# Performance work log

Measured on AMD Instinct MI355X. Metric: run time of the kernel, lower is better.

## Reference

```python
import jax, jax.numpy as jnp
import numpy as np
from jax import lax

B, L, D, C = 4096, 50, 128, 64
V = 100000
H = D // 2  # bidirectional LSTM hidden size; 2*H == emb_dim


def setup_inputs() -> dict:
    key = jax.random.key(0)
    ks = jax.random.split(key, 26)
    f = lambda k, s: jax.random.normal(k, s, dtype=jnp.float32) * 0.05
    return {
        "r_idx": jax.random.randint(ks[0], (B,), 0, V),
        "a_idx": jax.random.randint(ks[1], (B,), 0, V),
        "acc_idx": jax.random.randint(ks[2], (B,), 0, V),
        "rank_q": jax.random.normal(ks[3], (B, L, D), dtype=jnp.float32),
        "rank_q_len": jax.random.randint(ks[4], (B,), 0, L),
        "ru_emb": f(ks[5], (V, D)),
        "au_emb": f(ks[6], (V, D)),
        "Wih_f": f(ks[7], (4 * H, D)), "Whh_f": f(ks[8], (4 * H, H)),
        "bih_f": f(ks[9], (4 * H,)), "bhh_f": f(ks[10], (4 * H,)),
        "Wih_b": f(ks[11], (4 * H, D)), "Whh_b": f(ks[12], (4 * H, H)),
        "bih_b": f(ks[13], (4 * H,)), "bhh_b": f(ks[14], (4 * H,)),
        "conv1_w": f(ks[15], (C, 1, D)), "conv1_b": f(ks[16], (C,)),
        "conv2_w": f(ks[17], (C, 2, D)), "conv2_b": f(ks[18], (C,)),
        "conv3_w": f(ks[19], (C, 3, D)), "conv3_b": f(ks[20], (C,)),
        "fc1_w": f(ks[21], (6,)), "fc1_b": f(ks[22], (1,)),
        "fc2_w": f(ks[23], (C,)), "fc2_b": f(ks[24], (1,)),
    }


def _lstm_dir(x, Wih, Whh, bih, bhh, reverse):
    # x: [B, L, D] -> outputs [B, L, H]; PyTorch gate order i,f,g,o
    b = x.shape[0]
    xs = jnp.swapaxes(x, 0, 1)  # [L, B, D]
    h0 = jnp.zeros((b, Whh.shape[1]), x.dtype)

    def step(carry, xt):
        h, c = carry
        gates = xt @ Wih.T + h @ Whh.T + (bih + bhh)
        i, fg, g, o = jnp.split(gates, 4, axis=-1)
        i = jax.nn.sigmoid(i)
        fg = jax.nn.sigmoid(fg)
        g = jnp.tanh(g)
        o = jax.nn.sigmoid(o)
        c = fg * c + i * g
        h = o * jnp.tanh(c)
        return (h, c), h

    _, ys = lax.scan(step, (h0, h0), xs, reverse=reverse)
    return jnp.swapaxes(ys, 0, 1)


def _score(mat, conv1_w, conv1_b, conv2_w, conv2_b, conv3_w, conv3_b, fc1_w, fc1_b, fc2_w, fc2_b):
    # mat: [B, 3, D]; three tiny conv branches (kernel heights 1/2/3, width=D)
    branches = []
    for w, bias in ((conv1_w, conv1_b), (conv2_w, conv2_b), (conv3_w, conv3_b)):
        k = w.shape[1]
        wins = jnp.stack([mat[:, i:i + k] for i in range(3 - k + 1)], axis=1)  # [B, W, k, D]
        branches.append(jax.nn.relu(jnp.einsum('bwkd,ckd->bcw', wins, w) + bias[None, :, None]))
    s = jnp.concatenate(branches, axis=2)  # [B, C, 6]
    h = jnp.einsum('bcw,w->bc', s, fc1_w) + fc1_b[0]  # fc_new_1: 6 -> 1
    return jnp.einsum('bc,c->b', h, fc2_w) + fc2_b[0]  # fc_new_2: C -> 1


def reference(r_idx, a_idx, acc_idx, rank_q, rank_q_len, ru_emb, au_emb,
              Wih_f, Whh_f, bih_f, bhh_f, Wih_b, Whh_b, bih_b, bhh_b,
              conv1_w, conv1_b, conv2_w, conv2_b, conv3_w, conv3_b,
              fc1_w, fc1_b, fc2_w, fc2_b):
    emb_r = ru_emb[r_idx]
    emb_a = au_emb[a_idx]
    emb_acc = au_emb[acc_idx]
    # bidirectional LSTM over the question sequence
    out_f = _lstm_dir(rank_q, Wih_f, Whh_f, bih_f, bhh_f, reverse=False)
    out_b = _lstm_dir(rank_q, Wih_b, Whh_b, bih_b, bhh_b, reverse=True)
    q_out = jnp.concatenate([out_f, out_b], axis=-1)  # [B, L, D]
    # prepend a zero timestep, then gather per-example at index rank_q_len
    q_pad = jnp.concatenate([jnp.zeros((q_out.shape[0], 1, q_out.shape[2]), q_out.dtype), q_out], axis=1)
    emb_q = q_pad[jnp.arange(q_pad.shape[0]), rank_q_len]  # [B, D]
    low = jnp.stack([emb_r, emb_q, emb_a], axis=1)   # [B, 3, D]
    high = jnp.stack([emb_r, emb_q, emb_acc], axis=1)
    fcp = (conv1_w, conv1_b, conv2_w, conv2_b, conv3_w, conv3_b, fc1_w, fc1_b, fc2_w, fc2_b)
    low_s = _score(low, *fcp)
    high_s = _score(high, *fcp)
    return jnp.sum(low_s - high_s)
```

## Files before the change

kernel.cpp:

```cpp
#include <hip/hip_runtime.h>
#include <hip/hip_bf16.h>

#define LSEQ 50
#define BATCH 4096

typedef __attribute__((ext_vector_type(8))) short bf16x8;
typedef __attribute__((ext_vector_type(4))) float f32x4;

__device__ __forceinline__ unsigned cvtpk(float lo, float hi) {
    unsigned r;
    asm("v_cvt_pk_bf16_f32 %0, %1, %2" : "=v"(r) : "v"(lo), "v"(hi));
    return r;
}
__device__ __forceinline__ bf16x8 pack8(float4 a, float4 b) {
    uint4 u;
    u.x = cvtpk(a.x, a.y); u.y = cvtpk(a.z, a.w);
    u.z = cvtpk(b.x, b.y); u.w = cvtpk(b.z, b.w);
    return __builtin_bit_cast(bf16x8, u);
}
__device__ __forceinline__ float fsigm(float x) {
    return __builtin_amdgcn_rcpf(1.0f + __builtin_amdgcn_exp2f(-1.44269504f * x));
}
__device__ __forceinline__ float ftanh(float x) {
    float e = __builtin_amdgcn_exp2f(2.88539008f * x);
    return 1.0f - 2.0f * __builtin_amdgcn_rcpf(e + 1.0f);
}

__global__ __launch_bounds__(256, 2)
void lstm_kernel(const float* __restrict__ rank_q, const int* __restrict__ qlen,
                 const float* __restrict__ Wih_f, const float* __restrict__ Whh_f,
                 const float* __restrict__ bih_f, const float* __restrict__ bhh_f,
                 const float* __restrict__ Wih_b, const float* __restrict__ Whh_b,
                 const float* __restrict__ bih_b, const float* __restrict__ bhh_b,
                 float* __restrict__ embq)
{
    const int blk = blockIdx.x;
    const int dir = blk >> 8;
    const int b0  = (blk & 255) << 4;
    const int tid = threadIdx.x;
    const int wv  = tid >> 6;
    const int ln  = tid & 63;
    const int lm  = ln & 15;
    const int lq  = ln >> 4;
    const int m   = (wv << 4) + lm;

    const float* Wih = dir ? Wih_b : Wih_f;
    const float* Whh = dir ? Whh_b : Whh_f;
    const float* bih = dir ? bih_b : bih_f;
    const float* bhh = dir ? bhh_b : bhh_f;

    __shared__ __align__(16) unsigned short xbuf[3][16][136];
    __shared__ __align__(16) unsigned short hbuf[2][16][72];

    bf16x8 bfrag[4][6];
    float bias[4];
    #pragma unroll
    for (int j = 0; j < 4; ++j) {
        const int n = (j << 6) + m;
        bias[j] = bih[n] + bhh[n];
        #pragma unroll
        for (int s = 0; s < 6; ++s) {
            const int kb = (s << 5) + (lq << 3);
            const float* src = (s < 4) ? (Wih + n * 128 + kb)
                                       : (Whh + n * 64 + (kb - 128));
            bfrag[j][s] = pack8(*(const float4*)src, *(const float4*)(src + 4));
        }
    }

    int len_e[4];
    #pragma unroll
    for (int r = 0; r < 4; ++r) len_e[r] = qlen[b0 + (lq << 2) + r];

    float cst[4]  = {0.f, 0.f, 0.f, 0.f};
    float qval[4] = {0.f, 0.f, 0.f, 0.f};

    for (int i = tid; i < 16 * 72; i += 256) ((unsigned short*)hbuf)[i] = 0;

    const int se = tid >> 4;
    const int sd = (tid & 15) << 3;
    const int tstep = dir ? -128 : 128;
    const float* gp = rank_q + ((size_t)(b0 + se) * LSEQ + (dir ? LSEQ - 1 : 0)) * 128 + sd;

    {
        float4 a0 = *(const float4*)gp, b0v = *(const float4*)(gp + 4); gp += tstep;
        float4 a1 = *(const float4*)gp, b1v = *(const float4*)(gp + 4); gp += tstep;
        *(bf16x8*)&xbuf[0][se][sd] = pack8(a0, b0v);
        *(bf16x8*)&xbuf[1][se][sd] = pack8(a1, b1v);
    }
    __syncthreads();

    const int xoff = lm * 136 + (lq << 3);
    const int hoff = lm * 72 + (lq << 3);

    f32x4 accx[4];
    {
        const unsigned short* xb = &xbuf[0][0][0];
        bf16x8 x0 = *(const bf16x8*)(xb + xoff);
        bf16x8 x1 = *(const bf16x8*)(xb + xoff + 32);
        bf16x8 x2 = *(const bf16x8*)(xb + xoff + 64);
        bf16x8 x3 = *(const bf16x8*)(xb + xoff + 96);
        #pragma unroll
        for (int j = 0; j < 4; ++j) {
            f32x4 a = {bias[j], bias[j], bias[j], bias[j]};
            a = __builtin_amdgcn_mfma_f32_16x16x32_bf16(x0, bfrag[j][0], a, 0, 0, 0);
            a = __builtin_amdgcn_mfma_f32_16x16x32_bf16(x1, bfrag[j][1], a, 0, 0, 0);
            a = __builtin_amdgcn_mfma_f32_16x16x32_bf16(x2, bfrag[j][2], a, 0, 0, 0);
            a = __builtin_amdgcn_mfma_f32_16x16x32_bf16(x3, bfrag[j][3], a, 0, 0, 0);
            accx[j] = a;
        }
    }

    int r1 = 1, w2 = 2;
    for (int it = 0; it < LSEQ; ++it) {
        const int t   = dir ? (LSEQ - 1 - it) : it;
        const int rbh = it & 1;
        const int wbh = rbh ^ 1;

        float4 nxa, nxb;
        const bool pf = (it <= LSEQ - 3);
        if (pf) { nxa = *(const float4*)gp; nxb = *(const float4*)(gp + 4); gp += tstep; }

        const unsigned short* hb = &hbuf[rbh][0][0];
        bf16x8 ah0 = *(const bf16x8*)(hb + hoff);
        bf16x8 ah1 = *(const bf16x8*)(hb + hoff + 32);
        f32x4 gate[4];
        #pragma unroll
        for (int j = 0; j < 4; ++j) {
            f32x4 a = __builtin_amdgcn_mfma_f32_16x16x32_bf16(ah0, bfrag[j][4], accx[j], 0, 0, 0);
            gate[j]  = __builtin_amdgcn_mfma_f32_16x16x32_bf16(ah1, bfrag[j][5], a, 0, 0, 0);
        }

        if (it + 1 < LSEQ) {
            const unsigned short* xb = &xbuf[r1][0][0];
            bf16x8 x0 = *(const bf16x8*)(xb + xoff);
            bf16x8 x1 = *(const bf16x8*)(xb + xoff + 32);
            bf16x8 x2 = *(const bf16x8*)(xb + xoff + 64);
            bf16x8 x3 = *(const bf16x8*)(xb + xoff + 96);
            #pragma unroll
            for (int j = 0; j < 4; ++j) {
                f32x4 a = {bias[j], bias[j], bias[j], bias[j]};
                a = __builtin_amdgcn_mfma_f32_16x16x32_bf16(x0, bfrag[j][0], a, 0, 0, 0);
                a = __builtin_amdgcn_mfma_f32_16x16x32_bf16(x1, bfrag[j][1], a, 0, 0, 0);
                a = __builtin_amdgcn_mfma_f32_16x16x32_bf16(x2, bfrag[j][2], a, 0, 0, 0);
                a = __builtin_amdgcn_mfma_f32_16x16x32_bf16(x3, bfrag[j][3], a, 0, 0, 0);
                accx[j] = a;
            }
        }

        float hn[4];
        #pragma unroll
        for (int r = 0; r < 4; ++r) {
            float ig = fsigm(gate[0][r]);
            float fg = fsigm(gate[1][r]);
            float gg = ftanh(gate[2][r]);
            float og = fsigm(gate[3][r]);
            float cn = fg * cst[r] + ig * gg;
            cst[r] = cn;
            hn[r] = og * ftanh(cn);
            if (t == len_e[r] - 1) qval[r] = hn[r];
        }
        const unsigned u01 = cvtpk(hn[0], hn[1]);
        const unsigned u23 = cvtpk(hn[2], hn[3]);
        hbuf[wbh][(lq << 2) + 0][m] = (unsigned short)u01;
        hbuf[wbh][(lq << 2) + 1][m] = (unsigned short)(u01 >> 16);
        hbuf[wbh][(lq << 2) + 2][m] = (unsigned short)u23;
        hbuf[wbh][(lq << 2) + 3][m] = (unsigned short)(u23 >> 16);

        if (pf) *(bf16x8*)&xbuf[w2][se][sd] = pack8(nxa, nxb);

        __syncthreads();
        r1 = (r1 == 2) ? 0 : r1 + 1;
        w2 = (w2 == 2) ? 0 : w2 + 1;
    }

    #pragma unroll
    for (int r = 0; r < 4; ++r)
        embq[(size_t)(b0 + (lq << 2) + r) * 128 + (dir << 6) + m] = qval[r];
}

__global__ __launch_bounds__(256)
void prep_kernel(const float* __restrict__ c1w, const float* __restrict__ c2w,
                 const float* __restrict__ c3w, float* __restrict__ T)
{
    const int id = blockIdx.x * 256 + threadIdx.x;
    const int m  = id >> 13;
    const int rem = id & 8191;
    const int j  = rem >> 8;
    const int q  = rem & 255;
    const int c  = q >> 2;
    const int d  = (j << 2) + (q & 3);
    const float* src;
    switch (m) {
        case 0:  src = c1w + c * 128 + d;       break;
        case 1:  src = c2w + c * 256 + d;       break;
        case 2:  src = c2w + c * 256 + 128 + d; break;
        case 3:  src = c3w + c * 384 + d;       break;
        case 4:  src = c3w + c * 384 + 128 + d; break;
        default: src = c3w + c * 384 + 256 + d; break;
    }
    T[id] = *src;
}

__global__ __launch_bounds__(256)
void score_kernel(const int* __restrict__ r_idx, const int* __restrict__ a_idx,
                  const int* __restrict__ acc_idx,
                  const float* __restrict__ ru, const float* __restrict__ au,
                  const float* __restrict__ embq, const float* __restrict__ T,
                  const float* __restrict__ c1b, const float* __restrict__ c2b,
                  const float* __restrict__ c3b,
                  const float* __restrict__ fc1w, const float* __restrict__ fc2w,
                  float* __restrict__ diff)
{
    const int tid = threadIdx.x;
    const int wv  = tid >> 6;
    const int c   = tid & 63;
    const int b0  = blockIdx.x << 4;

    __shared__ __align__(16) float emb[64][132];
    {
        const int row = tid & 63;
        const int e   = row >> 2, v = row & 3;
        const int seg = (tid >> 6) << 5;
        const int bb  = b0 + e;
        const float* src = (v == 0) ? ru   + (size_t)r_idx[bb]   * 128 :
                           (v == 1) ? embq + (size_t)bb          * 128 :
                           (v == 2) ? au   + (size_t)a_idx[bb]   * 128 :
                                      au   + (size_t)acc_idx[bb] * 128;
        #pragma unroll
        for (int i = 0; i < 8; ++i) {
            float4 x = *(const float4*)(src + seg + (i << 2));
            *(float4*)&emb[row][seg + (i << 2)] = x;
        }
    }
    __syncthreads();

    float acc[4][9];
    #pragma unroll
    for (int e = 0; e < 4; ++e)
        #pragma unroll
        for (int k = 0; k < 9; ++k) acc[e][k] = 0.f;

    const float4* Tq = (const float4*)T;
    for (int j = 0; j < 32; ++j) {
        const float4* wq = Tq + j * 64 + c;
        const float4 w1  = wq[0];
        const float4 w20 = wq[2048];
        const float4 w21 = wq[4096];
        const float4 w30 = wq[6144];
        const float4 w31 = wq[8192];
        const float4 w32 = wq[10240];
        const int jd = j << 2;
        #pragma unroll
        for (int e = 0; e < 4; ++e) {
            const int br = ((wv << 2) + e) << 2;
            const float4 er = *(const float4*)&emb[br + 0][jd];
            const float4 eq = *(const float4*)&emb[br + 1][jd];
            const float4 ea = *(const float4*)&emb[br + 2][jd];
            const float4 ex = *(const float4*)&emb[br + 3][jd];
            acc[e][0] += w1.x*ea.x  + w1.y*ea.y  + w1.z*ea.z  + w1.w*ea.w;
            acc[e][1] += w1.x*ex.x  + w1.y*ex.y  + w1.z*ex.z  + w1.w*ex.w;
            acc[e][2] += w20.x*eq.x + w20.y*eq.y + w20.z*eq.z + w20.w*eq.w;
            acc[e][3] += w21.x*ea.x + w21.y*ea.y + w21.z*ea.z + w21.w*ea.w;
            acc[e][4] += w21.x*ex.x + w21.y*ex.y + w21.z*ex.z + w21.w*ex.w;
            acc[e][5] += w30.x*er.x + w30.y*er.y + w30.z*er.z + w30.w*er.w;
            acc[e][6] += w31.x*eq.x + w31.y*eq.y + w31.z*eq.z + w31.w*eq.w;
            acc[e][7] += w32.x*ea.x + w32.y*ea.y + w32.z*ea.z + w32.w*ea.w;
            acc[e][8] += w32.x*ex.x + w32.y*ex.y + w32.z*ex.z + w32.w*ex.w;
        }
    }

    const float b1 = c1b[c], b2 = c2b[c], b3 = c3b[c], f2 = fc2w[c];
    const float f12 = fc1w[2], f14 = fc1w[4], f15 = fc1w[5];
    #pragma unroll
    for (int e = 0; e < 4; ++e) {
        const float r1 = fmaxf(acc[e][0] + b1, 0.f) - fmaxf(acc[e][1] + b1, 0.f);
        const float r2 = fmaxf(acc[e][2] + acc[e][3] + b2, 0.f)
                       - fmaxf(acc[e][2] + acc[e][4] + b2, 0.f);
        const float r3 = fmaxf(acc[e][5] + acc[e][6] + acc[e][7] + b3, 0.f)
                       - fmaxf(acc[e][5] + acc[e][6] + acc[e][8] + b3, 0.f);
        float term = f2 * (f12 * r1 + f14 * r2 + f15 * r3);
        #pragma unroll
        for (int off = 32; off; off >>= 1) term += __shfl_down(term, off);
        if (c == 0) diff[b0 + (wv << 2) + e] = term;
    }
}

__global__ void reduce_kernel(const float* __restrict__ diff, float* __restrict__ out)
{
    __shared__ float s[256];
    const int tid = threadIdx.x;
    float v = 0.f;
    for (int i = tid; i < BATCH; i += 256) v += diff[i];
    s[tid] = v;
    __syncthreads();
    for (int st = 128; st > 0; st >>= 1) {
        if (tid < st) s[tid] += s[tid + st];
        __syncthreads();
    }
    if (tid == 0) out[0] = s[0];
}

extern "C" void kernel_launch(void* const* d_in, const int* in_sizes, int n_in,
                              void* d_out, int out_size, void* d_ws, size_t ws_size,
                              hipStream_t stream) {
    (void)in_sizes; (void)n_in; (void)out_size; (void)ws_size;
    const int*   r_idx   = (const int*)d_in[0];
    const int*   a_idx   = (const int*)d_in[1];
    const int*   acc_idx = (const int*)d_in[2];
    const float* rank_q  = (const float*)d_in[3];
    const int*   qlen    = (const int*)d_in[4];
    const float* ru      = (const float*)d_in[5];
    const float* au      = (const float*)d_in[6];
    const float* Wih_f   = (const float*)d_in[7];
    const float* Whh_f   = (const float*)d_in[8];
    const float* bih_f   = (const float*)d_in[9];
    const float* bhh_f   = (const float*)d_in[10];
    const float* Wih_b   = (const float*)d_in[11];
    const float* Whh_b   = (const float*)d_in[12];
    const float* bih_b   = (const float*)d_in[13];
    const float* bhh_b   = (const float*)d_in[14];
    const float* c1w     = (const float*)d_in[15];
    const float* c1b     = (const float*)d_in[16];
    const float* c2w     = (const float*)d_in[17];
    const float* c2b     = (const float*)d_in[18];
    const float* c3w     = (const float*)d_in[19];
    const float* c3b     = (const float*)d_in[20];
    const float* fc1w    = (const float*)d_in[21];
    const float* fc2w    = (const float*)d_in[23];

    float* embq = (float*)d_ws;
    float* diff = embq + (size_t)BATCH * 128;
    float* T    = diff + BATCH;

    prep_kernel<<<192, 256, 0, stream>>>(c1w, c2w, c3w, T);
    lstm_kernel<<<512, 256, 0, stream>>>(rank_q, qlen, Wih_f, Whh_f, bih_f, bhh_f,
                                         Wih_b, Whh_b, bih_b, bhh_b, embq);
    score_kernel<<<BATCH / 16, 256, 0, stream>>>(r_idx, a_idx, acc_idx, ru, au, embq, T,
                                                 c1b, c2b, c3b, fc1w, fc2w, diff);
    reduce_kernel<<<1, 256, 0, stream>>>(diff, (float*)d_out);
}
```

Measured before the change: 96.77 us.

## Sort batch by sequence length and truncate LSTM steps per group

A single-block counting sort orders batch elements by qlen, and each LSTM block handles 16 elements of similar length. The forward direction runs only up to the group's maximum length, and the backward direction runs only as far back as the smallest nonzero length. Blocks are interleaved short/long across the grid to balance load. Because only the hidden state at index len-1 is consumed, the skipped timesteps are never needed, so total recurrent work drops to roughly half. The cost is an extra serial sort kernel launch, gathered row loads of rank_q, and a scattered write of embq.

```diff
diff --git a/kernel.cpp b/kernel.cpp
--- a/kernel.cpp
+++ b/kernel.cpp
@@ -26,8 +26,29 @@
     return 1.0f - 2.0f * __builtin_amdgcn_rcpf(e + 1.0f);
 }
 
+__global__ __launch_bounds__(256)
+void sort_kernel(const int* __restrict__ qlen, int* __restrict__ perm)
+{
+    __shared__ int base[64];
+    const int tid = threadIdx.x;
+    if (tid < 64) base[tid] = 0;
+    __syncthreads();
+    for (int i = tid; i < BATCH; i += 256) atomicAdd(&base[qlen[i]], 1);
+    __syncthreads();
+    if (tid == 0) {
+        int s = 0;
+        for (int v = 0; v < 50; ++v) { int c = base[v]; base[v] = s; s += c; }
+    }
+    __syncthreads();
+    for (int i = tid; i < BATCH; i += 256) {
+        int pos = atomicAdd(&base[qlen[i]], 1);
+        perm[pos] = i;
+    }
+}
+
 __global__ __launch_bounds__(256, 2)
 void lstm_kernel(const float* __restrict__ rank_q, const int* __restrict__ qlen,
+                 const int* __restrict__ perm,
                  const float* __restrict__ Wih_f, const float* __restrict__ Whh_f,
                  const float* __restrict__ bih_f, const float* __restrict__ bhh_f,
                  const float* __restrict__ Wih_b, const float* __restrict__ Whh_b,
@@ -36,7 +57,9 @@
 {
     const int blk = blockIdx.x;
     const int dir = blk >> 8;
-    const int b0  = (blk & 255) << 4;
+    const int bb  = blk & 255;
+    const int grp = (bb & 1) ? (255 - (bb >> 1)) : (bb >> 1);
+    const int b0  = grp << 4;
     const int tid = threadIdx.x;
     const int wv  = tid >> 6;
     const int ln  = tid & 63;
@@ -51,6 +74,10 @@
 
     __shared__ __align__(16) unsigned short xbuf[3][16][136];
     __shared__ __align__(16) unsigned short hbuf[2][16][72];
+    __shared__ int len_s[16];
+
+    if (tid < 16) len_s[tid] = qlen[perm[b0 + tid]];
+    for (int i = tid; i < 16 * 72; i += 256) ((unsigned short*)hbuf)[i] = 0;
 
     bf16x8 bfrag[4][6];
     float bias[4];
@@ -67,71 +94,54 @@
         }
     }
 
-    int len_e[4];
-    #pragma unroll
-    for (int r = 0; r < 4; ++r) len_e[r] = qlen[b0 + (lq << 2) + r];
+    int exq[4], len_e[4];
+    #pragma unroll
+    for (int r = 0; r < 4; ++r) {
+        exq[r]   = perm[b0 + (lq << 2) + r];
+        len_e[r] = qlen[exq[r]];
+    }
 
     float cst[4]  = {0.f, 0.f, 0.f, 0.f};
     float qval[4] = {0.f, 0.f, 0.f, 0.f};
 
-    for (int i = tid; i < 16 * 72; i += 256) ((unsigned short*)hbuf)[i] = 0;
-
-    const int se = tid >> 4;
-    const int sd = (tid & 15) << 3;
+    const int se  = tid >> 4;
+    const int exs = perm[b0 + se];
+    const int sd  = (tid & 15) << 3;
     const int tstep = dir ? -128 : 128;
-    const float* gp = rank_q + ((size_t)(b0 + se) * LSEQ + (dir ? LSEQ - 1 : 0)) * 128 + sd;
-
-    {
-        float4 a0 = *(const float4*)gp, b0v = *(const float4*)(gp + 4); gp += tstep;
-        float4 a1 = *(const float4*)gp, b1v = *(const float4*)(gp + 4); gp += tstep;
-        *(bf16x8*)&xbuf[0][se][sd] = pack8(a0, b0v);
-        *(bf16x8*)&xbuf[1][se][sd] = pack8(a1, b1v);
-    }
-    __syncthreads();
-
-    const int xoff = lm * 136 + (lq << 3);
-    const int hoff = lm * 72 + (lq << 3);
-
-    f32x4 accx[4];
-    {
-        const unsigned short* xb = &xbuf[0][0][0];
-        bf16x8 x0 = *(const bf16x8*)(xb + xoff);
-        bf16x8 x1 = *(const bf16x8*)(xb + xoff + 32);
-        bf16x8 x2 = *(const bf16x8*)(xb + xoff + 64);
-        bf16x8 x3 = *(const bf16x8*)(xb + xoff + 96);
-        #pragma unroll
-        for (int j = 0; j < 4; ++j) {
-            f32x4 a = {bias[j], bias[j], bias[j], bias[j]};
-            a = __builtin_amdgcn_mfma_f32_16x16x32_bf16(x0, bfrag[j][0], a, 0, 0, 0);
-            a = __builtin_amdgcn_mfma_f32_16x16x32_bf16(x1, bfrag[j][1], a, 0, 0, 0);
-            a = __builtin_amdgcn_mfma_f32_16x16x32_bf16(x2, bfrag[j][2], a, 0, 0, 0);
-            a = __builtin_amdgcn_mfma_f32_16x16x32_bf16(x3, bfrag[j][3], a, 0, 0, 0);
-            accx[j] = a;
-        }
-    }
-
-    int r1 = 1, w2 = 2;
-    for (int it = 0; it < LSEQ; ++it) {
-        const int t   = dir ? (LSEQ - 1 - it) : it;
-        const int rbh = it & 1;
-        const int wbh = rbh ^ 1;
-
-        float4 nxa, nxb;
-        const bool pf = (it <= LSEQ - 3);
-        if (pf) { nxa = *(const float4*)gp; nxb = *(const float4*)(gp + 4); gp += tstep; }
-
-        const unsigned short* hb = &hbuf[rbh][0][0];
-        bf16x8 ah0 = *(const bf16x8*)(hb + hoff);
-        bf16x8 ah1 = *(const bf16x8*)(hb + hoff + 32);
-        f32x4 gate[4];
-        #pragma unroll
-        for (int j = 0; j < 4; ++j) {
-            f32x4 a = __builtin_amdgcn_mfma_f32_16x16x32_bf16(ah0, bfrag[j][4], accx[j], 0, 0, 0);
-            gate[j]  = __builtin_amdgcn_mfma_f32_16x16x32_bf16(ah1, bfrag[j][5], a, 0, 0, 0);
-        }
-
-        if (it + 1 < LSEQ) {
-            const unsigned short* xb = &xbuf[r1][0][0];
+    const float* gp = rank_q + ((size_t)exs * LSEQ + (dir ? LSEQ - 1 : 0)) * 128 + sd;
+
+    __syncthreads();
+
+    int steps;
+    if (dir == 0) {
+        int mx = 0;
+        #pragma unroll
+        for (int i = 0; i < 16; ++i) mx = max(mx, len_s[i]);
+        steps = mx;
+    } else {
+        int mn = 51;
+        #pragma unroll
+        for (int i = 0; i < 16; ++i) { int l = len_s[i]; mn = min(mn, l ? l : 51); }
+        steps = (mn == 51) ? 0 : 51 - mn;
+    }
+
+    if (steps > 0) {
+        {
+            float4 a0 = *(const float4*)gp, b0v = *(const float4*)(gp + 4); gp += tstep;
+            float4 a1 = *(const float4*)gp, b1v = *(const float4*)(gp + 4); gp += tstep;
+            *(bf16x8*)&xbuf[0][se][sd] = pack8(a0, b0v);
+            *(bf16x8*)&xbuf[1][se][sd] = pack8(a1, b1v);
+        }
+        float4 ha, hb2;
+        if (3 <= steps) { ha = *(const float4*)gp; hb2 = *(const float4*)(gp + 4); gp += tstep; }
+        __syncthreads();
+
+        const int xoff = lm * 136 + (lq << 3);
+        const int hoff = lm * 72 + (lq << 3);
+
+        f32x4 accx[4];
+        {
+            const unsigned short* xb = &xbuf[0][0][0];
             bf16x8 x0 = *(const bf16x8*)(xb + xoff);
             bf16x8 x1 = *(const bf16x8*)(xb + xoff + 32);
             bf16x8 x2 = *(const bf16x8*)(xb + xoff + 64);
@@ -147,35 +157,74 @@
             }
         }
 
-        float hn[4];
-        #pragma unroll
-        for (int r = 0; r < 4; ++r) {
-            float ig = fsigm(gate[0][r]);
-            float fg = fsigm(gate[1][r]);
-            float gg = ftanh(gate[2][r]);
-            float og = fsigm(gate[3][r]);
-            float cn = fg * cst[r] + ig * gg;
-            cst[r] = cn;
-            hn[r] = og * ftanh(cn);
-            if (t == len_e[r] - 1) qval[r] = hn[r];
-        }
-        const unsigned u01 = cvtpk(hn[0], hn[1]);
-        const unsigned u23 = cvtpk(hn[2], hn[3]);
-        hbuf[wbh][(lq << 2) + 0][m] = (unsigned short)u01;
-        hbuf[wbh][(lq << 2) + 1][m] = (unsigned short)(u01 >> 16);
-        hbuf[wbh][(lq << 2) + 2][m] = (unsigned short)u23;
-        hbuf[wbh][(lq << 2) + 3][m] = (unsigned short)(u23 >> 16);
-
-        if (pf) *(bf16x8*)&xbuf[w2][se][sd] = pack8(nxa, nxb);
-
-        __syncthreads();
-        r1 = (r1 == 2) ? 0 : r1 + 1;
-        w2 = (w2 == 2) ? 0 : w2 + 1;
+        int r1 = 1, w2 = 2;
+        for (int it = 0; it < steps; ++it) {
+            const int t   = dir ? (LSEQ - 1 - it) : it;
+            const int rbh = it & 1;
+            const int wbh = rbh ^ 1;
+
+            float4 na, nb;
+            const bool nv = (it + 4 <= steps);
+            if (nv) { na = *(const float4*)gp; nb = *(const float4*)(gp + 4); gp += tstep; }
+
+            const unsigned short* hb = &hbuf[rbh][0][0];
+            bf16x8 ah0 = *(const bf16x8*)(hb + hoff);
+            bf16x8 ah1 = *(const bf16x8*)(hb + hoff + 32);
+            f32x4 gate[4];
+            #pragma unroll
+            for (int j = 0; j < 4; ++j) {
+                f32x4 a = __builtin_amdgcn_mfma_f32_16x16x32_bf16(ah0, bfrag[j][4], accx[j], 0, 0, 0);
+                gate[j]  = __builtin_amdgcn_mfma_f32_16x16x32_bf16(ah1, bfrag[j][5], a, 0, 0, 0);
+            }
+
+            if (it + 1 < steps) {
+                const unsigned short* xb = &xbuf[r1][0][0];
+                bf16x8 x0 = *(const bf16x8*)(xb + xoff);
+                bf16x8 x1 = *(const bf16x8*)(xb + xoff + 32);
+                bf16x8 x2 = *(const bf16x8*)(xb + xoff + 64);
+                bf16x8 x3 = *(const bf16x8*)(xb + xoff + 96);
+                #pragma unroll
+                for (int j = 0; j < 4; ++j) {
+                    f32x4 a = {bias[j], bias[j], bias[j], bias[j]};
+                    a = __builtin_amdgcn_mfma_f32_16x16x32_bf16(x0, bfrag[j][0], a, 0, 0, 0);
+                    a = __builtin_amdgcn_mfma_f32_16x16x32_bf16(x1, bfrag[j][1], a, 0, 0, 0);
+                    a = __builtin_amdgcn_mfma_f32_16x16x32_bf16(x2, bfrag[j][2], a, 0, 0, 0);
+                    a = __builtin_amdgcn_mfma_f32_16x16x32_bf16(x3, bfrag[j][3], a, 0, 0, 0);
+                    accx[j] = a;
+                }
+            }
+
+            float hn[4];
+            #pragma unroll
+            for (int r = 0; r < 4; ++r) {
+                float ig = fsigm(gate[0][r]);
+                float fg = fsigm(gate[1][r]);
+                float gg = ftanh(gate[2][r]);
+                float og = fsigm(gate[3][r]);
+                float cn = fg * cst[r] + ig * gg;
+                cst[r] = cn;
+                hn[r] = og * ftanh(cn);
+                if (t == len_e[r] - 1) qval[r] = hn[r];
+            }
+            const unsigned u01 = cvtpk(hn[0], hn[1]);
+            const unsigned u23 = cvtpk(hn[2], hn[3]);
+            hbuf[wbh][(lq << 2) + 0][m] = (unsigned short)u01;
+            hbuf[wbh][(lq << 2) + 1][m] = (unsigned short)(u01 >> 16);
+            hbuf[wbh][(lq << 2) + 2][m] = (unsigned short)u23;
+            hbuf[wbh][(lq << 2) + 3][m] = (unsigned short)(u23 >> 16);
+
+            if (it + 3 <= steps) *(bf16x8*)&xbuf[w2][se][sd] = pack8(ha, hb2);
+            ha = na; hb2 = nb;
+
+            __syncthreads();
+            r1 = (r1 == 2) ? 0 : r1 + 1;
+            w2 = (w2 == 2) ? 0 : w2 + 1;
+        }
     }
 
     #pragma unroll
     for (int r = 0; r < 4; ++r)
-        embq[(size_t)(b0 + (lq << 2) + r) * 128 + (dir << 6) + m] = qval[r];
+        embq[(size_t)exq[r] * 128 + (dir << 6) + m] = qval[r];
 }
 
 __global__ __launch_bounds__(256)
@@ -331,9 +380,12 @@
     float* embq = (float*)d_ws;
     float* diff = embq + (size_t)BATCH * 128;
     float* T    = diff + BATCH;
-
+    int*   perm = (int*)(T + 49152);
+
+    sort_kernel<<<1, 256, 0, stream>>>(qlen, perm);
     prep_kernel<<<192, 256, 0, stream>>>(c1w, c2w, c3w, T);
-    lstm_kernel<<<512, 256, 0, stream>>>(rank_q, qlen, Wih_f, Whh_f, bih_f, bhh_f,
+    lstm_kernel<<<512, 256, 0, stream>>>(rank_q, qlen, perm,
+                                         Wih_f, Whh_f, bih_f, bhh_f,
                                          Wih_b, Whh_b, bih_b, bhh_b, embq);
     score_kernel<<<BATCH / 16, 256, 0, stream>>>(r_idx, a_idx, acc_idx, ru, au, embq, T,
                                                  c1b, c2b, c3b, fc1w, fc2w, diff);
```

After: 95.26 us. Within noise of the previous version (-1.6%).

## Deepen rank_q prefetch ring and use raw barrier in LSTM recurrence

Applied to the files above, without the earlier changes.

The shared x staging ring grows from 3 to 4 slots. Two register-held prefetch sets now keep global loads of rank_q about six timesteps ahead, and the time loop is manually unrolled by two through a macro. The per-step __syncthreads is replaced with an inline `s_waitcnt lgkmcnt(0); s_barrier`, so the barrier waits only on LDS traffic and in-flight global loads are not drained every step. This aims to hide global load latency behind the serial recurrence, at the cost of more registers and more LDS per block.

```diff
diff --git a/kernel.cpp b/kernel.cpp
--- a/kernel.cpp
+++ b/kernel.cpp
@@ -49,7 +49,7 @@
     const float* bih = dir ? bih_b : bih_f;
     const float* bhh = dir ? bhh_b : bhh_f;
 
-    __shared__ __align__(16) unsigned short xbuf[3][16][136];
+    __shared__ __align__(16) unsigned short xbuf[4][16][136];
     __shared__ __align__(16) unsigned short hbuf[2][16][72];
 
     bf16x8 bfrag[4][6];
@@ -81,12 +81,16 @@
     const int tstep = dir ? -128 : 128;
     const float* gp = rank_q + ((size_t)(b0 + se) * LSEQ + (dir ? LSEQ - 1 : 0)) * 128 + sd;
 
-    {
-        float4 a0 = *(const float4*)gp, b0v = *(const float4*)(gp + 4); gp += tstep;
-        float4 a1 = *(const float4*)gp, b1v = *(const float4*)(gp + 4); gp += tstep;
-        *(bf16x8*)&xbuf[0][se][sd] = pack8(a0, b0v);
-        *(bf16x8*)&xbuf[1][se][sd] = pack8(a1, b1v);
-    }
+    float4 p0a = *(const float4*)gp, p0b = *(const float4*)(gp + 4); gp += tstep;
+    float4 p1a = *(const float4*)gp, p1b = *(const float4*)(gp + 4); gp += tstep;
+    float4 p2a = *(const float4*)gp, p2b = *(const float4*)(gp + 4); gp += tstep;
+    float4 p3a = *(const float4*)gp, p3b = *(const float4*)(gp + 4); gp += tstep;
+    float4 fa0 = *(const float4*)gp, fa1 = *(const float4*)(gp + 4); gp += tstep;
+    float4 fb0 = *(const float4*)gp, fb1 = *(const float4*)(gp + 4); gp += tstep;
+    *(bf16x8*)&xbuf[0][se][sd] = pack8(p0a, p0b);
+    *(bf16x8*)&xbuf[1][se][sd] = pack8(p1a, p1b);
+    *(bf16x8*)&xbuf[2][se][sd] = pack8(p2a, p2b);
+    *(bf16x8*)&xbuf[3][se][sd] = pack8(p3a, p3b);
     __syncthreads();
 
     const int xoff = lm * 136 + (lq << 3);
@@ -110,68 +114,75 @@
         }
     }
 
-    int r1 = 1, w2 = 2;
-    for (int it = 0; it < LSEQ; ++it) {
-        const int t   = dir ? (LSEQ - 1 - it) : it;
-        const int rbh = it & 1;
-        const int wbh = rbh ^ 1;
-
-        float4 nxa, nxb;
-        const bool pf = (it <= LSEQ - 3);
-        if (pf) { nxa = *(const float4*)gp; nxb = *(const float4*)(gp + 4); gp += tstep; }
-
-        const unsigned short* hb = &hbuf[rbh][0][0];
-        bf16x8 ah0 = *(const bf16x8*)(hb + hoff);
-        bf16x8 ah1 = *(const bf16x8*)(hb + hoff + 32);
-        f32x4 gate[4];
-        #pragma unroll
-        for (int j = 0; j < 4; ++j) {
-            f32x4 a = __builtin_amdgcn_mfma_f32_16x16x32_bf16(ah0, bfrag[j][4], accx[j], 0, 0, 0);
-            gate[j]  = __builtin_amdgcn_mfma_f32_16x16x32_bf16(ah1, bfrag[j][5], a, 0, 0, 0);
-        }
-
-        if (it + 1 < LSEQ) {
-            const unsigned short* xb = &xbuf[r1][0][0];
-            bf16x8 x0 = *(const bf16x8*)(xb + xoff);
-            bf16x8 x1 = *(const bf16x8*)(xb + xoff + 32);
-            bf16x8 x2 = *(const bf16x8*)(xb + xoff + 64);
-            bf16x8 x3 = *(const bf16x8*)(xb + xoff + 96);
-            #pragma unroll
-            for (int j = 0; j < 4; ++j) {
-                f32x4 a = {bias[j], bias[j], bias[j], bias[j]};
-                a = __builtin_amdgcn_mfma_f32_16x16x32_bf16(x0, bfrag[j][0], a, 0, 0, 0);
-                a = __builtin_amdgcn_mfma_f32_16x16x32_bf16(x1, bfrag[j][1], a, 0, 0, 0);
-                a = __builtin_amdgcn_mfma_f32_16x16x32_bf16(x2, bfrag[j][2], a, 0, 0, 0);
-                a = __builtin_amdgcn_mfma_f32_16x16x32_bf16(x3, bfrag[j][3], a, 0, 0, 0);
-                accx[j] = a;
-            }
-        }
-
-        float hn[4];
-        #pragma unroll
-        for (int r = 0; r < 4; ++r) {
-            float ig = fsigm(gate[0][r]);
-            float fg = fsigm(gate[1][r]);
-            float gg = ftanh(gate[2][r]);
-            float og = fsigm(gate[3][r]);
-            float cn = fg * cst[r] + ig * gg;
-            cst[r] = cn;
-            hn[r] = og * ftanh(cn);
-            if (t == len_e[r] - 1) qval[r] = hn[r];
-        }
-        const unsigned u01 = cvtpk(hn[0], hn[1]);
-        const unsigned u23 = cvtpk(hn[2], hn[3]);
-        hbuf[wbh][(lq << 2) + 0][m] = (unsigned short)u01;
-        hbuf[wbh][(lq << 2) + 1][m] = (unsigned short)(u01 >> 16);
-        hbuf[wbh][(lq << 2) + 2][m] = (unsigned short)u23;
-        hbuf[wbh][(lq << 2) + 3][m] = (unsigned short)(u23 >> 16);
-
-        if (pf) *(bf16x8*)&xbuf[w2][se][sd] = pack8(nxa, nxb);
-
-        __syncthreads();
-        r1 = (r1 == 2) ? 0 : r1 + 1;
-        w2 = (w2 == 2) ? 0 : w2 + 1;
-    }
+#define LSTM_BODY(T, FS0, FS1)                                                  \
+    {                                                                           \
+        const int t  = (T);                                                     \
+        const int rb = t & 1, wb = rb ^ 1;                                      \
+             \
+        if (t + 4 < LSEQ) *(bf16x8*)&xbuf[t & 3][se][sd] = pack8(FS0, FS1);     \
+                \
+        if (t + 6 < LSEQ) {                                                     \
+            FS0 = *(const float4*)gp; FS1 = *(const float4*)(gp + 4);           \
+            gp += tstep;                                                        \
+        }                                                                       \
+                       \
+        const unsigned short* hb = &hbuf[rb][0][0];                             \
+        bf16x8 ah0 = *(const bf16x8*)(hb + hoff);                               \
+        bf16x8 ah1 = *(const bf16x8*)(hb + hoff + 32);                          \
+        f32x4 gate[4];                                                          \
+        _Pragma("unroll")                                                       \
+        for (int j = 0; j < 4; ++j) {                                           \
+            f32x4 a = __builtin_amdgcn_mfma_f32_16x16x32_bf16(                  \
+                          ah0, bfrag[j][4], accx[j], 0, 0, 0);                  \
+            gate[j] = __builtin_amdgcn_mfma_f32_16x16x32_bf16(                  \
+                          ah1, bfrag[j][5], a, 0, 0, 0);                        \
+        }                                                                       \
+          \
+        if (t + 1 < LSEQ) {                                                     \
+            const unsigned short* xb = &xbuf[(t + 1) & 3][0][0];                \
+            bf16x8 x0 = *(const bf16x8*)(xb + xoff);                            \
+            bf16x8 x1 = *(const bf16x8*)(xb + xoff + 32);                       \
+            bf16x8 x2 = *(const bf16x8*)(xb + xoff + 64);                       \
+            bf16x8 x3 = *(const bf16x8*)(xb + xoff + 96);                       \
+            _Pragma("unroll")                                                   \
+            for (int j = 0; j < 4; ++j) {                                       \
+                f32x4 a = {bias[j], bias[j], bias[j], bias[j]};                 \
+                a = __builtin_amdgcn_mfma_f32_16x16x32_bf16(x0, bfrag[j][0], a, 0, 0, 0); \
+                a = __builtin_amdgcn_mfma_f32_16x16x32_bf16(x1, bfrag[j][1], a, 0, 0, 0); \
+                a = __builtin_amdgcn_mfma_f32_16x16x32_bf16(x2, bfrag[j][2], a, 0, 0, 0); \
+                a = __builtin_amdgcn_mfma_f32_16x16x32_bf16(x3, bfrag[j][3], a, 0, 0, 0); \
+                accx[j] = a;                                                    \
+            }                                                                   \
+        }                                                                       \
+                                  \
+        const int tcap = dir ? (LSEQ - 1 - t) : t;                              \
+        float hn[4];                                                            \
+        _Pragma("unroll")                                                       \
+        for (int r = 0; r < 4; ++r) {                                           \
+            float ig = fsigm(gate[0][r]);                                       \
+            float fg = fsigm(gate[1][r]);                                       \
+            float gg = ftanh(gate[2][r]);                                       \
+            float og = fsigm(gate[3][r]);                                       \
+            float cn = fg * cst[r] + ig * gg;                                   \
+            cst[r] = cn;                                                        \
+            hn[r] = og * ftanh(cn);                                             \
+            if (tcap == len_e[r] - 1) qval[r] = hn[r];                          \
+        }                                                                       \
+        const unsigned u01 = cvtpk(hn[0], hn[1]);                               \
+        const unsigned u23 = cvtpk(hn[2], hn[3]);                               \
+        hbuf[wb][(lq << 2) + 0][m] = (unsigned short)u01;                       \
+        hbuf[wb][(lq << 2) + 1][m] = (unsigned short)(u01 >> 16);               \
+        hbuf[wb][(lq << 2) + 2][m] = (unsigned short)u23;                       \
+        hbuf[wb][(lq << 2) + 3][m] = (unsigned short)(u23 >> 16);               \
+                    \
+        asm volatile("s_waitcnt lgkmcnt(0)\n\ts_barrier" ::: "memory");         \
+    }
+
+    for (int i = 0; i < LSEQ / 2; ++i) {
+        LSTM_BODY(2 * i,     fa0, fa1)
+        LSTM_BODY(2 * i + 1, fb0, fb1)
+    }
+#undef LSTM_BODY
 
     #pragma unroll
     for (int r = 0; r < 4; ++r)
```

Result: no change. 98.20 us (+1.5%).
